# Kernel tuning notes

Hardware: AMD Instinct MI355X
Metric: run time of the kernel (lower is better)

Reference implementation:

```python
import jax, jax.numpy as jnp
import numpy as np

L1, L2, ALPHA, BETA, EPS = 0.5, 1.5, 1.0, 50000000.0, 1e-08


def tube(att, label):
    # per-row cosine/sine TUBE distance, fully vectorized over batch
    dot = jnp.sum(att * label, axis=-1)            # [B]
    p_norm = jnp.sqrt(jnp.sum(att * att, axis=-1))
    g_norm = jnp.sqrt(jnp.sum(label * label, axis=-1))
    denom = p_norm * g_norm
    cosine = jnp.where(denom == 0, 0.0, dot / jnp.where(denom == 0, 1.0, denom))
    s_s = 1.0 - jnp.square(cosine)
    # s_s < 0 -> sine = 0 ; s_s == 0 -> sqrt(s_s + eps) ; else sqrt(s_s)
    sine = jnp.where(s_s < 0, 0.0, jnp.sqrt(jnp.where(s_s <= 0, EPS, s_s)))
    r_all = p_norm * cosine / jnp.where(g_norm == 0, g_norm + EPS, g_norm)
    base = p_norm * sine + jnp.abs(g_norm - p_norm * cosine)
    ds = jnp.where(r_all >= 1, L1 * base,
         jnp.where(r_all >= 0, base,
                   L2 * jnp.abs(p_norm * cosine - g_norm - p_norm * sine)))
    ds = -jnp.log(jnp.tanh(1.0 / ds))
    return jnp.mean(ds)


def kl_loss(mu, logvar):
    return -0.5 * BETA * jnp.mean(1.0 + logvar - jnp.square(mu) - jnp.exp(logvar))


def cross_entropy(logits, label_idx):
    logp = jax.nn.log_softmax(logits, axis=-1)
    return -jnp.mean(jnp.take_along_axis(logp, label_idx[:, None], axis=1)[:, 0])


def setup_inputs() -> dict:
    key = jax.random.key(0)
    ks = jax.random.split(key, 12)
    B, C, D, Z = 16384, 100, 512, 128
    return {
        "fusion_out": jax.random.normal(ks[0], (B, C), jnp.float32),
        "comple_out": jax.random.normal(ks[1], (B, D), jnp.float32),
        "labels": jax.random.normal(ks[2], (B, C), jnp.float32),
        "labels_encoder": jax.random.normal(ks[3], (B, D), jnp.float32),
        "x_A": jax.random.normal(ks[4], (B, D), jnp.float32),
        "x_A_reconstructed": jax.random.normal(ks[5], (B, D), jnp.float32),
        "x_B": jax.random.normal(ks[6], (B, D), jnp.float32),
        "x_B_reconstructed": jax.random.normal(ks[7], (B, D), jnp.float32),
        "x_C": jax.random.normal(ks[8], (B, D), jnp.float32),
        "x_C_reconstructed": jax.random.normal(ks[9], (B, D), jnp.float32),
        "mu": jax.random.normal(ks[10], (B, Z), jnp.float32),
        "logvar": jax.random.normal(ks[11], (B, Z), jnp.float32),
    }


def reference(fusion_out, comple_out, labels, labels_encoder, x_A,
              x_A_reconstructed, x_B, x_B_reconstructed, x_C,
              x_C_reconstructed, mu, logvar):
    label_idx = jnp.argmax(labels, axis=1)
    tube_A = ALPHA * tube(x_A_reconstructed, x_A)
    tube_B = ALPHA * tube(x_B_reconstructed, x_B)
    tube_C = ALPHA * tube(x_C_reconstructed, x_C)
    kl = kl_loss(mu, logvar)
    st_all = ALPHA * tube(comple_out, labels_encoder)
    ce = cross_entropy(fusion_out, label_idx)
    return tube_A + tube_B + tube_C + kl + ce + st_all
```

## Files before the change

kernel.cpp:

```cpp
#include <hip/hip_runtime.h>
#include <math.h>

static constexpr float kL1   = 0.5f;
static constexpr float kL2   = 1.5f;
static constexpr float kBeta = 50000000.0f;
static constexpr float kEps  = 1e-08f;

__device__ __forceinline__ float waveSum(float v) {
#pragma unroll
    for (int off = 32; off > 0; off >>= 1) v += __shfl_xor(v, off, 64);
    return v;
}

__device__ __forceinline__ float tubeTail(float dot, float pp, float gg) {
    float p_norm = sqrtf(pp);
    float g_norm = sqrtf(gg);
    float denom  = p_norm * g_norm;
    float cosine = (denom == 0.0f) ? 0.0f : dot / denom;
    float s_s    = 1.0f - cosine * cosine;
    float sine   = (s_s < 0.0f) ? 0.0f : sqrtf((s_s <= 0.0f) ? kEps : s_s);
    float gd     = (g_norm == 0.0f) ? (g_norm + kEps) : g_norm;
    float pc     = p_norm * cosine;
    float r_all  = pc / gd;
    float base   = p_norm * sine + fabsf(g_norm - pc);
    float ds     = (r_all >= 1.0f) ? (kL1 * base)
                 : ((r_all >= 0.0f) ? base
                                    : kL2 * fabsf(pc - g_norm - p_norm * sine));
    float t  = 1.0f / ds;
    float em = __expf(-2.0f * t);
    return __logf(1.0f + em) - __logf(fmaxf(1.0f - em, 1e-30f));
}

#define ACC3(A, L)                                        \
    dot += A.x*L.x + A.y*L.y + A.z*L.z + A.w*L.w;         \
    pp  += A.x*A.x + A.y*A.y + A.z*A.z + A.w*A.w;         \
    gg  += L.x*L.x + L.y*L.y + L.z*L.z + L.w*L.w;

__global__ __launch_bounds__(256) void fused_loss_partials(
    const float* __restrict__ fusion_out, const float* __restrict__ comple_out,
    const float* __restrict__ labels,     const float* __restrict__ labels_enc,
    const float* __restrict__ xA,  const float* __restrict__ xAr,
    const float* __restrict__ xB,  const float* __restrict__ xBr,
    const float* __restrict__ xC,  const float* __restrict__ xCr,
    const float* __restrict__ mu,  const float* __restrict__ logvar,
    float* __restrict__ partials,
    int C, int Z, int tubeBlocks, int klBlocks)
{
    const int lane = threadIdx.x & 63;
    const int wave = threadIdx.x >> 6;
    const int bid  = blockIdx.x;
    constexpr int B = 16384;
    constexpr int D = 512;

    float my = 0.0f;

    if (bid < tubeBlocks) {
        const int t   = bid * 4 + wave;
        const int h   = lane >> 5;
        const int sub = lane & 31;
        const int p   = t >> 13;
        const int r   = (2 * t) & (B - 1);
        const float* ab = (p == 0) ? xAr : (p == 1) ? xBr : (p == 2) ? xCr : comple_out;
        const float* lb = (p == 0) ? xA  : (p == 1) ? xB  : (p == 2) ? xC  : labels_enc;
        const float4* a = (const float4*)(ab + (size_t)r * D) + (h * 128 + sub);
        const float4* l = (const float4*)(lb + (size_t)r * D) + (h * 128 + sub);
        float4 A0 = a[0], A1 = a[32], A2 = a[64], A3 = a[96];
        float4 L0 = l[0], L1 = l[32], L2 = l[64], L3 = l[96];
        float dot = 0.0f, pp = 0.0f, gg = 0.0f;
        ACC3(A0, L0); ACC3(A1, L1); ACC3(A2, L2); ACC3(A3, L3);
#pragma unroll
        for (int off = 16; off > 0; off >>= 1) {
            dot += __shfl_xor(dot, off, 64);
            pp  += __shfl_xor(pp,  off, 64);
            gg  += __shfl_xor(gg,  off, 64);
        }
        my = tubeTail(dot, pp, gg) * (1.0f / (32.0f * (float)B));
    } else if (bid < tubeBlocks + klBlocks) {
        const int tid = (bid - tubeBlocks) * 256 + threadIdx.x;
        const float4 m = ((const float4*)mu)[tid];
        const float4 l = ((const float4*)logvar)[tid];
        float acc = (1.0f + l.x - m.x * m.x - __expf(l.x))
                  + (1.0f + l.y - m.y * m.y - __expf(l.y))
                  + (1.0f + l.z - m.z * m.z - __expf(l.z))
                  + (1.0f + l.w - m.w * m.w - __expf(l.w));
        my = acc * (-0.5f * kBeta / ((float)B * (float)Z));
    } else {
        const int r = (bid - tubeBlocks - klBlocks) * 4 + wave;
        const float* lrow = labels     + (size_t)r * C;
        const float* frow = fusion_out + (size_t)r * C;
        const bool has0 = (lane < C);
        const bool has1 = (lane + 64 < C);
        float v0 = has0 ? lrow[lane]      : -INFINITY;
        float v1 = has1 ? lrow[lane + 64] : -INFINITY;
        float f0 = has0 ? frow[lane]      : -INFINITY;
        float f1 = has1 ? frow[lane + 64] : -INFINITY;
        float bv; int bi;
        if (v1 > v0) { bv = v1; bi = lane + 64; } else { bv = v0; bi = lane; }
#pragma unroll
        for (int off = 32; off > 0; off >>= 1) {
            float ov = __shfl_xor(bv, off, 64);
            int   oi = __shfl_xor(bi, off, 64);
            if (ov > bv || (ov == bv && oi < bi)) { bv = ov; bi = oi; }
        }
        float m = fmaxf(f0, f1);
#pragma unroll
        for (int off = 32; off > 0; off >>= 1) m = fmaxf(m, __shfl_xor(m, off, 64));
        float e = 0.0f;
        if (has0) e += __expf(f0 - m);
        if (has1) e += __expf(f1 - m);
        e = waveSum(e);
        float tgt = (bi < 64) ? __shfl(f0, bi, 64) : __shfl(f1, bi - 64, 64);
        if (lane == 0) my = -(tgt - m - __logf(e)) / (float)B;
    }

    float s = waveSum(my);
    __shared__ float sw[4];
    if (lane == 0) sw[wave] = s;
    __syncthreads();
    if (threadIdx.x == 0)
        partials[bid] = sw[0] + sw[1] + sw[2] + sw[3];
}

__global__ __launch_bounds__(256) void reduce_partials(
    const float* __restrict__ partials, float* __restrict__ out, int n)
{
    float s = 0.0f;
    for (int i = threadIdx.x; i < n; i += 256) s += partials[i];
    s = waveSum(s);
    __shared__ float sw[4];
    const int lane = threadIdx.x & 63;
    const int wave = threadIdx.x >> 6;
    if (lane == 0) sw[wave] = s;
    __syncthreads();
    if (threadIdx.x == 0) out[0] = sw[0] + sw[1] + sw[2] + sw[3];
}

extern "C" void kernel_launch(void* const* d_in, const int* in_sizes, int n_in,
                              void* d_out, int out_size, void* d_ws, size_t ws_size,
                              hipStream_t stream) {
    const float* fusion_out = (const float*)d_in[0];
    const float* comple_out = (const float*)d_in[1];
    const float* labels     = (const float*)d_in[2];
    const float* labels_enc = (const float*)d_in[3];
    const float* xA  = (const float*)d_in[4];
    const float* xAr = (const float*)d_in[5];
    const float* xB  = (const float*)d_in[6];
    const float* xBr = (const float*)d_in[7];
    const float* xC  = (const float*)d_in[8];
    const float* xCr = (const float*)d_in[9];
    const float* mu  = (const float*)d_in[10];
    const float* lv  = (const float*)d_in[11];
    float* out = (float*)d_out;
    float* ws  = (float*)d_ws;

    const int B = 16384;
    const int C = in_sizes[0] / B;
    const int Z = in_sizes[10] / B;

    const int tubeBlocks = (4 * B / 2) / 4;
    const int klBlocks   = (B * Z / 4) / 256;
    const int ceBlocks   = B / 4;
    const int totalBlocks = tubeBlocks + klBlocks + ceBlocks;

    fused_loss_partials<<<totalBlocks, 256, 0, stream>>>(
        fusion_out, comple_out, labels, labels_enc,
        xA, xAr, xB, xBr, xC, xCr, mu, lv,
        ws, C, Z, tubeBlocks, klBlocks);
    reduce_partials<<<1, 256, 0, stream>>>(ws, out, totalBlocks);
}
```

Baseline: 291.6 us.

## Increase per-wave loads in flight for tube and KL sections

The tube section now uses a grid-stride loop over fewer blocks. Each wave processes four rows per iteration and issues sixteen 16-byte loads per lane up front, with an empty asm barrier that keeps all loads issued before any use. The KL section has each thread handle two float4 pairs, halving its block count, and the kernel gains a min-blocks-per-CU launch bound. The aim is more memory-level parallelism and less block scheduling overhead, at the cost of higher register pressure and fewer resident waves.

```diff
diff --git a/kernel.cpp b/kernel.cpp
--- a/kernel.cpp
+++ b/kernel.cpp
@@ -5,6 +5,8 @@
 static constexpr float kL2   = 1.5f;
 static constexpr float kBeta = 50000000.0f;
 static constexpr float kEps  = 1e-08f;
+
+typedef float f32x4 __attribute__((ext_vector_type(4)));
 
 __device__ __forceinline__ float waveSum(float v) {
 #pragma unroll
@@ -31,12 +33,12 @@
     return __logf(1.0f + em) - __logf(fmaxf(1.0f - em, 1e-30f));
 }
 
-#define ACC3(A, L)                                        \
+#define ACC3(dot, pp, gg, A, L)                           \
     dot += A.x*L.x + A.y*L.y + A.z*L.z + A.w*L.w;         \
     pp  += A.x*A.x + A.y*A.y + A.z*A.z + A.w*A.w;         \
     gg  += L.x*L.x + L.y*L.y + L.z*L.z + L.w*L.w;
 
-__global__ __launch_bounds__(256) void fused_loss_partials(
+__global__ __launch_bounds__(256, 2) void fused_loss_partials(
     const float* __restrict__ fusion_out, const float* __restrict__ comple_out,
     const float* __restrict__ labels,     const float* __restrict__ labels_enc,
     const float* __restrict__ xA,  const float* __restrict__ xAr,
@@ -55,34 +57,67 @@
     float my = 0.0f;
 
     if (bid < tubeBlocks) {
-        const int t   = bid * 4 + wave;
         const int h   = lane >> 5;
         const int sub = lane & 31;
-        const int p   = t >> 13;
-        const int r   = (2 * t) & (B - 1);
-        const float* ab = (p == 0) ? xAr : (p == 1) ? xBr : (p == 2) ? xCr : comple_out;
-        const float* lb = (p == 0) ? xA  : (p == 1) ? xB  : (p == 2) ? xC  : labels_enc;
-        const float4* a = (const float4*)(ab + (size_t)r * D) + (h * 128 + sub);
-        const float4* l = (const float4*)(lb + (size_t)r * D) + (h * 128 + sub);
-        float4 A0 = a[0], A1 = a[32], A2 = a[64], A3 = a[96];
-        float4 L0 = l[0], L1 = l[32], L2 = l[64], L3 = l[96];
-        float dot = 0.0f, pp = 0.0f, gg = 0.0f;
-        ACC3(A0, L0); ACC3(A1, L1); ACC3(A2, L2); ACC3(A3, L3);
-#pragma unroll
-        for (int off = 16; off > 0; off >>= 1) {
-            dot += __shfl_xor(dot, off, 64);
-            pp  += __shfl_xor(pp,  off, 64);
-            gg  += __shfl_xor(gg,  off, 64);
+        const int nQuads = B;
+        const int gw = bid * 4 + wave;
+        const int tw = tubeBlocks * 4;
+        float acc = 0.0f;
+        for (int q = gw; q < nQuads; q += tw) {
+            const int p = q >> 12;
+            const int r = (q << 2) & (B - 1);
+            const float* ab = (p == 0) ? xAr : (p == 1) ? xBr : (p == 2) ? xCr : comple_out;
+            const float* lb = (p == 0) ? xA  : (p == 1) ? xB  : (p == 2) ? xC  : labels_enc;
+            const f32x4* a0 = (const f32x4*)(ab + (size_t)r * D) + (h * 128 + sub);
+            const f32x4* l0 = (const f32x4*)(lb + (size_t)r * D) + (h * 128 + sub);
+            const f32x4* a1 = a0 + 256;
+            const f32x4* l1 = l0 + 256;
+
+            f32x4 A0 = a0[0], A1 = a0[32], A2 = a0[64], A3 = a0[96];
+            f32x4 L0 = l0[0], L1 = l0[32], L2 = l0[64], L3 = l0[96];
+            f32x4 A4 = a1[0], A5 = a1[32], A6 = a1[64], A7 = a1[96];
+            f32x4 L4 = l1[0], L5 = l1[32], L6 = l1[64], L7 = l1[96];
+            asm volatile("" ::
+                "v"(A0), "v"(A1), "v"(A2), "v"(A3),
+                "v"(L0), "v"(L1), "v"(L2), "v"(L3),
+                "v"(A4), "v"(A5), "v"(A6), "v"(A7),
+                "v"(L4), "v"(L5), "v"(L6), "v"(L7));
+
+            float dot0 = 0.0f, pp0 = 0.0f, gg0 = 0.0f;
+            float dot1 = 0.0f, pp1 = 0.0f, gg1 = 0.0f;
+            ACC3(dot0, pp0, gg0, A0, L0); ACC3(dot0, pp0, gg0, A1, L1);
+            ACC3(dot0, pp0, gg0, A2, L2); ACC3(dot0, pp0, gg0, A3, L3);
+            ACC3(dot1, pp1, gg1, A4, L4); ACC3(dot1, pp1, gg1, A5, L5);
+            ACC3(dot1, pp1, gg1, A6, L6); ACC3(dot1, pp1, gg1, A7, L7);
+
+#pragma unroll
+            for (int off = 16; off > 0; off >>= 1) {
+                dot0 += __shfl_xor(dot0, off, 64);
+                pp0  += __shfl_xor(pp0,  off, 64);
+                gg0  += __shfl_xor(gg0,  off, 64);
+                dot1 += __shfl_xor(dot1, off, 64);
+                pp1  += __shfl_xor(pp1,  off, 64);
+                gg1  += __shfl_xor(gg1,  off, 64);
+            }
+            acc += tubeTail(dot0, pp0, gg0);
+            acc += tubeTail(dot1, pp1, gg1);
         }
-        my = tubeTail(dot, pp, gg) * (1.0f / (32.0f * (float)B));
+        my = acc * (1.0f / (32.0f * (float)B));
     } else if (bid < tubeBlocks + klBlocks) {
-        const int tid = (bid - tubeBlocks) * 256 + threadIdx.x;
-        const float4 m = ((const float4*)mu)[tid];
-        const float4 l = ((const float4*)logvar)[tid];
-        float acc = (1.0f + l.x - m.x * m.x - __expf(l.x))
-                  + (1.0f + l.y - m.y * m.y - __expf(l.y))
-                  + (1.0f + l.z - m.z * m.z - __expf(l.z))
-                  + (1.0f + l.w - m.w * m.w - __expf(l.w));
+        const int base = (bid - tubeBlocks) * 512 + threadIdx.x;
+        const int i0 = base, i1 = base + 256;
+        const f32x4* mu4 = (const f32x4*)mu;
+        const f32x4* lv4 = (const f32x4*)logvar;
+        f32x4 m0 = mu4[i0], l0 = lv4[i0], m1 = mu4[i1], l1 = lv4[i1];
+        asm volatile("" :: "v"(m0), "v"(l0), "v"(m1), "v"(l1));
+        float acc = (1.0f + l0.x - m0.x * m0.x - __expf(l0.x))
+                  + (1.0f + l0.y - m0.y * m0.y - __expf(l0.y))
+                  + (1.0f + l0.z - m0.z * m0.z - __expf(l0.z))
+                  + (1.0f + l0.w - m0.w * m0.w - __expf(l0.w))
+                  + (1.0f + l1.x - m1.x * m1.x - __expf(l1.x))
+                  + (1.0f + l1.y - m1.y * m1.y - __expf(l1.y))
+                  + (1.0f + l1.z - m1.z * m1.z - __expf(l1.z))
+                  + (1.0f + l1.w - m1.w * m1.w - __expf(l1.w));
         my = acc * (-0.5f * kBeta / ((float)B * (float)Z));
     } else {
         const int r = (bid - tubeBlocks - klBlocks) * 4 + wave;
@@ -157,8 +192,8 @@
     const int C = in_sizes[0] / B;
     const int Z = in_sizes[10] / B;
 
-    const int tubeBlocks = (4 * B / 2) / 4;
-    const int klBlocks   = (B * Z / 4) / 256;
+    const int tubeBlocks = 2048;
+    const int klBlocks   = (B * Z / 4) / 512;
     const int ceBlocks   = B / 4;
     const int totalBlocks = tubeBlocks + klBlocks + ceBlocks;
 
```

Result: no change. 294.3 us (+0.9%).

## Software-pipeline tube loads with inline-asm double buffering and fewer blocks

Applied to the files above, without the earlier changes.

Each tube wave now processes 16 rows instead of 2, issuing global_load_dwordx4 through inline asm into two register buffers. Manual s_waitcnt vmcnt controls when each buffer is consumed, so loads for the next row pair overlap compute on the current one. The tube grid shrinks to 1024 blocks, and KL blocks each handle two float4 per thread. This aims to raise memory-level parallelism and cut per-block overhead, at the cost of higher register use, fewer waves and fragile hand-written asm ordering.

```diff
diff --git a/kernel.cpp b/kernel.cpp
--- a/kernel.cpp
+++ b/kernel.cpp
@@ -5,6 +5,9 @@
 static constexpr float kL2   = 1.5f;
 static constexpr float kBeta = 50000000.0f;
 static constexpr float kEps  = 1e-08f;
+
+typedef float f32x4 __attribute__((ext_vector_type(4)));
+typedef unsigned long long u64;
 
 __device__ __forceinline__ float waveSum(float v) {
 #pragma unroll
@@ -31,10 +34,45 @@
     return __logf(1.0f + em) - __logf(fmaxf(1.0f - em, 1e-30f));
 }
 
-#define ACC3(A, L)                                        \
+#define ACC3(dot, pp, gg, A, L)                           \
     dot += A.x*L.x + A.y*L.y + A.z*L.z + A.w*L.w;         \
     pp  += A.x*A.x + A.y*A.y + A.z*A.z + A.w*A.w;         \
     gg  += L.x*L.x + L.y*L.y + L.z*L.z + L.w*L.w;
+
+#define TLOAD(d0,d1,d2,d3,e0,e1,e2,e3, av, lv)                       \
+    asm volatile(                                                    \
+        "global_load_dwordx4 %0, %8, off\n\t"                        \
+        "global_load_dwordx4 %1, %8, off offset:512\n\t"             \
+        "global_load_dwordx4 %2, %8, off offset:1024\n\t"            \
+        "global_load_dwordx4 %3, %8, off offset:1536\n\t"            \
+        "global_load_dwordx4 %4, %9, off\n\t"                        \
+        "global_load_dwordx4 %5, %9, off offset:512\n\t"             \
+        "global_load_dwordx4 %6, %9, off offset:1024\n\t"            \
+        "global_load_dwordx4 %7, %9, off offset:1536\n\t"            \
+        : "=&v"(d0), "=&v"(d1), "=&v"(d2), "=&v"(d3),                \
+          "=&v"(e0), "=&v"(e1), "=&v"(e2), "=&v"(e3)                 \
+        : "v"(av), "v"(lv))
+
+#define VMWAIT8() do { asm volatile("s_waitcnt vmcnt(8)");                    \
+                       __builtin_amdgcn_sched_barrier(0); } while (0)
+#define VMWAIT0() do { asm volatile("s_waitcnt vmcnt(0)");                    \
+                       __builtin_amdgcn_sched_barrier(0); } while (0)
+
+__device__ __forceinline__ void tubeCompute(
+    f32x4 a0, f32x4 a1, f32x4 a2, f32x4 a3,
+    f32x4 l0, f32x4 l1, f32x4 l2, f32x4 l3, float& acc)
+{
+    float dot = 0.0f, pp = 0.0f, gg = 0.0f;
+    ACC3(dot, pp, gg, a0, l0); ACC3(dot, pp, gg, a1, l1);
+    ACC3(dot, pp, gg, a2, l2); ACC3(dot, pp, gg, a3, l3);
+#pragma unroll
+    for (int off = 16; off > 0; off >>= 1) {
+        dot += __shfl_xor(dot, off, 64);
+        pp  += __shfl_xor(pp,  off, 64);
+        gg  += __shfl_xor(gg,  off, 64);
+    }
+    acc += tubeTail(dot, pp, gg);
+}
 
 __global__ __launch_bounds__(256) void fused_loss_partials(
     const float* __restrict__ fusion_out, const float* __restrict__ comple_out,
@@ -55,34 +93,52 @@
     float my = 0.0f;
 
     if (bid < tubeBlocks) {
-        const int t   = bid * 4 + wave;
         const int h   = lane >> 5;
         const int sub = lane & 31;
-        const int p   = t >> 13;
-        const int r   = (2 * t) & (B - 1);
+        const int gw  = bid * 4 + wave;
+        const int p   = gw >> 10;
+        const int idx0 = (gw & 1023) * 8;
         const float* ab = (p == 0) ? xAr : (p == 1) ? xBr : (p == 2) ? xCr : comple_out;
         const float* lb = (p == 0) ? xA  : (p == 1) ? xB  : (p == 2) ? xC  : labels_enc;
-        const float4* a = (const float4*)(ab + (size_t)r * D) + (h * 128 + sub);
-        const float4* l = (const float4*)(lb + (size_t)r * D) + (h * 128 + sub);
-        float4 A0 = a[0], A1 = a[32], A2 = a[64], A3 = a[96];
-        float4 L0 = l[0], L1 = l[32], L2 = l[64], L3 = l[96];
-        float dot = 0.0f, pp = 0.0f, gg = 0.0f;
-        ACC3(A0, L0); ACC3(A1, L1); ACC3(A2, L2); ACC3(A3, L3);
-#pragma unroll
-        for (int off = 16; off > 0; off >>= 1) {
-            dot += __shfl_xor(dot, off, 64);
-            pp  += __shfl_xor(pp,  off, 64);
-            gg  += __shfl_xor(gg,  off, 64);
-        }
-        my = tubeTail(dot, pp, gg) * (1.0f / (32.0f * (float)B));
+        const u64 aB = (u64)(const void*)ab + (u64)(2 * idx0 + h) * (D * 4) + (u64)sub * 16;
+        const u64 lB = (u64)(const void*)lb + (u64)(2 * idx0 + h) * (D * 4) + (u64)sub * 16;
+
+        f32x4 aA0, aA1, aA2, aA3, lA0, lA1, lA2, lA3;
+        f32x4 aB0, aB1, aB2, aB3, lB0, lB1, lB2, lB3;
+        float acc = 0.0f;
+
+        TLOAD(aA0,aA1,aA2,aA3,lA0,lA1,lA2,lA3, aB + 0ull*4096, lB + 0ull*4096);
+        TLOAD(aB0,aB1,aB2,aB3,lB0,lB1,lB2,lB3, aB + 1ull*4096, lB + 1ull*4096);
+        VMWAIT8(); tubeCompute(aA0,aA1,aA2,aA3,lA0,lA1,lA2,lA3, acc);
+        TLOAD(aA0,aA1,aA2,aA3,lA0,lA1,lA2,lA3, aB + 2ull*4096, lB + 2ull*4096);
+        VMWAIT8(); tubeCompute(aB0,aB1,aB2,aB3,lB0,lB1,lB2,lB3, acc);
+        TLOAD(aB0,aB1,aB2,aB3,lB0,lB1,lB2,lB3, aB + 3ull*4096, lB + 3ull*4096);
+        VMWAIT8(); tubeCompute(aA0,aA1,aA2,aA3,lA0,lA1,lA2,lA3, acc);
+        TLOAD(aA0,aA1,aA2,aA3,lA0,lA1,lA2,lA3, aB + 4ull*4096, lB + 4ull*4096);
+        VMWAIT8(); tubeCompute(aB0,aB1,aB2,aB3,lB0,lB1,lB2,lB3, acc);
+        TLOAD(aB0,aB1,aB2,aB3,lB0,lB1,lB2,lB3, aB + 5ull*4096, lB + 5ull*4096);
+        VMWAIT8(); tubeCompute(aA0,aA1,aA2,aA3,lA0,lA1,lA2,lA3, acc);
+        TLOAD(aA0,aA1,aA2,aA3,lA0,lA1,lA2,lA3, aB + 6ull*4096, lB + 6ull*4096);
+        VMWAIT8(); tubeCompute(aB0,aB1,aB2,aB3,lB0,lB1,lB2,lB3, acc);
+        TLOAD(aB0,aB1,aB2,aB3,lB0,lB1,lB2,lB3, aB + 7ull*4096, lB + 7ull*4096);
+        VMWAIT8(); tubeCompute(aA0,aA1,aA2,aA3,lA0,lA1,lA2,lA3, acc);
+        VMWAIT0(); tubeCompute(aB0,aB1,aB2,aB3,lB0,lB1,lB2,lB3, acc);
+
+        my = acc * (1.0f / (32.0f * (float)B));
     } else if (bid < tubeBlocks + klBlocks) {
-        const int tid = (bid - tubeBlocks) * 256 + threadIdx.x;
-        const float4 m = ((const float4*)mu)[tid];
-        const float4 l = ((const float4*)logvar)[tid];
-        float acc = (1.0f + l.x - m.x * m.x - __expf(l.x))
-                  + (1.0f + l.y - m.y * m.y - __expf(l.y))
-                  + (1.0f + l.z - m.z * m.z - __expf(l.z))
-                  + (1.0f + l.w - m.w * m.w - __expf(l.w));
+        const int base = (bid - tubeBlocks) * 512 + threadIdx.x;
+        const int i0 = base, i1 = base + 256;
+        const f32x4* mu4 = (const f32x4*)mu;
+        const f32x4* lv4 = (const f32x4*)logvar;
+        f32x4 m0 = mu4[i0], l0 = lv4[i0], m1 = mu4[i1], l1 = lv4[i1];
+        float acc = (1.0f + l0.x - m0.x * m0.x - __expf(l0.x))
+                  + (1.0f + l0.y - m0.y * m0.y - __expf(l0.y))
+                  + (1.0f + l0.z - m0.z * m0.z - __expf(l0.z))
+                  + (1.0f + l0.w - m0.w * m0.w - __expf(l0.w))
+                  + (1.0f + l1.x - m1.x * m1.x - __expf(l1.x))
+                  + (1.0f + l1.y - m1.y * m1.y - __expf(l1.y))
+                  + (1.0f + l1.z - m1.z * m1.z - __expf(l1.z))
+                  + (1.0f + l1.w - m1.w * m1.w - __expf(l1.w));
         my = acc * (-0.5f * kBeta / ((float)B * (float)Z));
     } else {
         const int r = (bid - tubeBlocks - klBlocks) * 4 + wave;
@@ -157,8 +213,8 @@
     const int C = in_sizes[0] / B;
     const int Z = in_sizes[10] / B;
 
-    const int tubeBlocks = (4 * B / 2) / 4;
-    const int klBlocks   = (B * Z / 4) / 256;
+    const int tubeBlocks = 1024;
+    const int klBlocks   = (B * Z / 4) / 512;
     const int ceBlocks   = B / 4;
     const int totalBlocks = tubeBlocks + klBlocks + ceBlocks;
 
```

Result: no change. 291.9 us (+0.1%).
